# Optimization experiments

Hardware: AMD Instinct MI355X
Metric: run time of the kernel (lower is better)

Reference implementation:

```python
import jax, jax.numpy as jnp
import numpy as np

AH, AW = 7, 7            # alignedHeight, alignedWidth
SCALE = 0.0625           # spatialScale = 1/16


def setup_inputs() -> dict:
    key = jax.random.key(0)
    k1, k2, k3, k4 = jax.random.split(key, 4)
    B, C, H, W, K = 4, 1024, 50, 50, 512
    features = jax.random.normal(k1, (B, C, H, W), dtype=jnp.float32)
    bidx = jax.random.randint(k2, (K, 1), 0, B).astype(jnp.float32)
    xs = jnp.sort(jax.random.uniform(k3, (K, 2), minval=0.0, maxval=799.0), axis=1)
    ys = jnp.sort(jax.random.uniform(k4, (K, 2), minval=0.0, maxval=799.0), axis=1)
    # rois: (batch_idx, x1, y1, x2, y2) in image coords
    rois = jnp.concatenate([bidx, xs[:, 0:1], ys[:, 0:1], xs[:, 1:2], ys[:, 1:2]], axis=1)
    return {"features": features, "rois": rois}


def _roi_align(features, rois):
    # legacy roi_align: grid of (AH+1)x(AW+1) points, bin = extent/(grid-1),
    # one bilinear sample per grid point, zero outside feature map.
    B, C, H, W = features.shape
    bidx = rois[:, 0].astype(jnp.int32)
    x1 = rois[:, 1] * SCALE
    y1 = rois[:, 2] * SCALE
    x2 = rois[:, 3] * SCALE
    y2 = rois[:, 4] * SCALE
    bh = jnp.maximum(y2 - y1, 0.0) / AH  # (AH+1)-1 grid intervals
    bw = jnp.maximum(x2 - x1, 0.0) / AW
    ys = y1[:, None] + jnp.arange(AH + 1, dtype=jnp.float32) * bh[:, None]  # [K,AH+1]
    xs = x1[:, None] + jnp.arange(AW + 1, dtype=jnp.float32) * bw[:, None]  # [K,AW+1]
    yg = ys[:, :, None]   # [K,AH+1,1]
    xg = xs[:, None, :]   # [K,1,AW+1]
    valid = (yg >= 0) & (yg < H) & (xg >= 0) & (xg < W)   # [K,AH+1,AW+1]
    y0 = jnp.clip(jnp.floor(yg), 0, H - 2).astype(jnp.int32)
    x0 = jnp.clip(jnp.floor(xg), 0, W - 2).astype(jnp.int32)
    wy = yg - y0.astype(jnp.float32)  # [K,AH+1,1]
    wx = xg - x0.astype(jnp.float32)  # [K,1,AW+1]
    b = bidx[:, None, None]
    # gathered corners: [K, AH+1, AW+1, C]
    v00 = features[b, :, y0, x0]
    v01 = features[b, :, y0, x0 + 1]
    v10 = features[b, :, y0 + 1, x0]
    v11 = features[b, :, y0 + 1, x0 + 1]
    out = (v00 * ((1 - wy) * (1 - wx))[..., None]
           + v01 * ((1 - wy) * wx)[..., None]
           + v10 * (wy * (1 - wx))[..., None]
           + v11 * (wy * wx)[..., None])
    out = jnp.where(valid[..., None], out, 0.0)
    return jnp.transpose(out, (0, 3, 1, 2))  # [K, C, AH+1, AW+1]


def reference(features, rois):
    a = _roi_align(features, rois)
    # avg_pool2d(kernel=2, stride=1) -> [K, C, AH, AW]
    pooled = (a[..., :-1, :-1] + a[..., 1:, :-1] + a[..., :-1, 1:] + a[..., 1:, 1:]) * 0.25
    return pooled
```

## Files before the change

kernel.cpp:

```cpp
#include <hip/hip_runtime.h>

#define K_ROIS   512
#define BATCH    4
#define CHANNELS 1024
#define FH       50
#define FW       50
#define AH       7
#define AW       7
#define SCALE_F  0.0625f
#define CPT      4


__global__ void roi_prep(const float* __restrict__ rois,
                         int* __restrict__ cnt,
                         int* __restrict__ list,
                         float4* __restrict__ params) {
    int r = blockIdx.x * blockDim.x + threadIdx.x;
    if (r >= K_ROIS) return;
    float bf = rois[r * 5 + 0];
    float x1 = rois[r * 5 + 1] * SCALE_F;
    float y1 = rois[r * 5 + 2] * SCALE_F;
    float x2 = rois[r * 5 + 3] * SCALE_F;
    float y2 = rois[r * 5 + 4] * SCALE_F;
    float bw = fmaxf(x2 - x1, 0.f) * (1.f / (float)AW);
    float bh = fmaxf(y2 - y1, 0.f) * (1.f / (float)AH);
    params[r] = make_float4(x1, y1, bw, bh);
    int ib = (int)bf;
    int pos = atomicAdd(&cnt[ib], 1);
    list[ib * K_ROIS + pos] = r;
}

__global__ __launch_bounds__(256)
void roi_pool(const float* __restrict__ feat,
              const int* __restrict__ cnt,
              const int* __restrict__ list,
              const float4* __restrict__ params,
              float* __restrict__ out) {
    __shared__ float4 patch4[CPT * FH * FW / 4];
    float* patch = (float*)patch4;

    const int b  = blockIdx.x & 3;
    const int c0 = (blockIdx.x >> 2) * CPT;

    const float4* src = (const float4*)(feat + ((size_t)b * CHANNELS + c0) * (FH * FW));
    for (int idx = threadIdx.x; idx < CPT * FH * FW / 4; idx += 256)
        patch4[idx] = src[idx];
    __syncthreads();

    const int lane = threadIdx.x & 63;
    const int wv   = threadIdx.x >> 6;
    const int j = lane >> 3;
    const int i = lane & 7;
    const float jf = (float)j;
    const float iff = (float)i;
    const bool do_out = (j < AH) && (i < AW);
    const int outoff = j * AW + i;

    const int n = cnt[b];
    for (int rr = wv; rr < n; rr += 4) {
        const int roi = list[b * K_ROIS + rr];
        const float4 p = params[roi];
        const float xg = fmaf(iff, p.z, p.x);
        const float yg = fmaf(jf, p.w, p.y);
        const bool valid = (yg >= 0.f) && (yg < (float)FH) &&
                           (xg >= 0.f) && (xg < (float)FW);
        const float y0f = fminf(fmaxf(floorf(yg), 0.f), (float)(FH - 2));
        const float x0f = fminf(fmaxf(floorf(xg), 0.f), (float)(FW - 2));
        const float wy = yg - y0f;
        const float wx = xg - x0f;
        const float omwy = 1.f - wy;
        const float omwx = 1.f - wx;
        float w00 = omwy * omwx;
        float w01 = omwy * wx;
        float w10 = wy * omwx;
        float w11 = wy * wx;
        if (!valid) { w00 = 0.f; w01 = 0.f; w10 = 0.f; w11 = 0.f; }
        const int addr = (int)y0f * FW + (int)x0f;
        const size_t obase = (size_t)roi * (CHANNELS * AH * AW)
                           + (size_t)c0 * (AH * AW) + outoff;
        #pragma unroll
        for (int ch = 0; ch < CPT; ++ch) {
            const int a = ch * (FH * FW) + addr;
            const float v00 = patch[a];
            const float v01 = patch[a + 1];
            const float v10 = patch[a + FW];
            const float v11 = patch[a + FW + 1];
            float s = w00 * v00 + w01 * v01 + w10 * v10 + w11 * v11;
            float s1 = s + __shfl_down(s, 1);
            float s2 = s1 + __shfl_down(s1, 8);
            if (do_out)
                out[obase + (size_t)ch * (AH * AW)] = s2 * 0.25f;
        }
    }
}

extern "C" void kernel_launch(void* const* d_in, const int* in_sizes, int n_in,
                              void* d_out, int out_size, void* d_ws, size_t ws_size,
                              hipStream_t stream) {
    const float* feat = (const float*)d_in[0];
    const float* rois = (const float*)d_in[1];
    float* out = (float*)d_out;

    char* ws = (char*)d_ws;
    int* cnt      = (int*)ws;
    int* list     = (int*)(ws + 16);
    float4* params = (float4*)(ws + 16 + 4 * K_ROIS * sizeof(int));

    hipMemsetAsync(cnt, 0, 16, stream);
    roi_prep<<<2, 256, 0, stream>>>(rois, cnt, list, params);
    roi_pool<<<BATCH * (CHANNELS / CPT), 256, 0, stream>>>(feat, cnt, list, params, out);
}
```

Baseline: 160.2 us.

## Interleave channels in shared patch as float4 and prefetch sorted ROI params

The shared-memory patch is now stored channel-interleaved as one float4 per pixel, so each bilinear corner is a single 128-bit LDS read covering all four channels instead of four scalar reads. ROI parameters are written directly in per-batch sorted order by the prep kernel, removing the indirect params[roi] lookup, and the next ROI's parameters are software-prefetched one iteration ahead. The global load into shared memory becomes four scalar strided loads per pixel instead of coalesced float4 loads, which may cost more on the staging side. Workspace usage grows because params are now sized per batch slot.

```diff
diff --git a/kernel.cpp b/kernel.cpp
--- a/kernel.cpp
+++ b/kernel.cpp
@@ -13,8 +13,8 @@
 
 __global__ void roi_prep(const float* __restrict__ rois,
                          int* __restrict__ cnt,
-                         int* __restrict__ list,
-                         float4* __restrict__ params) {
+                         int* __restrict__ roiIdx,
+                         float4* __restrict__ paramsS) {
     int r = blockIdx.x * blockDim.x + threadIdx.x;
     if (r >= K_ROIS) return;
     float bf = rois[r * 5 + 0];
@@ -24,27 +24,32 @@
     float y2 = rois[r * 5 + 4] * SCALE_F;
     float bw = fmaxf(x2 - x1, 0.f) * (1.f / (float)AW);
     float bh = fmaxf(y2 - y1, 0.f) * (1.f / (float)AH);
-    params[r] = make_float4(x1, y1, bw, bh);
     int ib = (int)bf;
     int pos = atomicAdd(&cnt[ib], 1);
-    list[ib * K_ROIS + pos] = r;
+    roiIdx[ib * K_ROIS + pos] = r;
+    paramsS[ib * K_ROIS + pos] = make_float4(x1, y1, bw, bh);
 }
 
 __global__ __launch_bounds__(256)
 void roi_pool(const float* __restrict__ feat,
               const int* __restrict__ cnt,
-              const int* __restrict__ list,
-              const float4* __restrict__ params,
+              const int* __restrict__ roiIdx,
+              const float4* __restrict__ paramsS,
               float* __restrict__ out) {
-    __shared__ float4 patch4[CPT * FH * FW / 4];
-    float* patch = (float*)patch4;
+    __shared__ float4 patch4[FH * FW];
 
     const int b  = blockIdx.x & 3;
     const int c0 = (blockIdx.x >> 2) * CPT;
 
-    const float4* src = (const float4*)(feat + ((size_t)b * CHANNELS + c0) * (FH * FW));
-    for (int idx = threadIdx.x; idx < CPT * FH * FW / 4; idx += 256)
-        patch4[idx] = src[idx];
+    const float* pl = feat + ((size_t)b * CHANNELS + c0) * (FH * FW);
+    for (int idx = threadIdx.x; idx < FH * FW; idx += 256) {
+        float4 v;
+        v.x = pl[idx];
+        v.y = pl[idx + FH * FW];
+        v.z = pl[idx + 2 * FH * FW];
+        v.w = pl[idx + 3 * FH * FW];
+        patch4[idx] = v;
+    }
     __syncthreads();
 
     const int lane = threadIdx.x & 63;
@@ -57,11 +62,21 @@
     const int outoff = j * AW + i;
 
     const int n = cnt[b];
-    for (int rr = wv; rr < n; rr += 4) {
-        const int roi = list[b * K_ROIS + rr];
-        const float4 p = params[roi];
-        const float xg = fmaf(iff, p.z, p.x);
-        const float yg = fmaf(jf, p.w, p.y);
+    const int base = b * K_ROIS;
+
+    int rr = wv;
+    float4 pp = make_float4(0.f, 0.f, 0.f, 0.f);
+    int roi = 0;
+    if (rr < n) { pp = paramsS[base + rr]; roi = roiIdx[base + rr]; }
+
+    while (rr < n) {
+        const int rn = rr + 4;
+        float4 ppn = pp;
+        int roin = roi;
+        if (rn < n) { ppn = paramsS[base + rn]; roin = roiIdx[base + rn]; }
+
+        const float xg = fmaf(iff, pp.z, pp.x);
+        const float yg = fmaf(jf, pp.w, pp.y);
         const bool valid = (yg >= 0.f) && (yg < (float)FH) &&
                            (xg >= 0.f) && (xg < (float)FW);
         const float y0f = fminf(fmaxf(floorf(yg), 0.f), (float)(FH - 2));
@@ -75,22 +90,39 @@
         float w10 = wy * omwx;
         float w11 = wy * wx;
         if (!valid) { w00 = 0.f; w01 = 0.f; w10 = 0.f; w11 = 0.f; }
-        const int addr = (int)y0f * FW + (int)x0f;
-        const size_t obase = (size_t)roi * (CHANNELS * AH * AW)
-                           + (size_t)c0 * (AH * AW) + outoff;
-        #pragma unroll
-        for (int ch = 0; ch < CPT; ++ch) {
-            const int a = ch * (FH * FW) + addr;
-            const float v00 = patch[a];
-            const float v01 = patch[a + 1];
-            const float v10 = patch[a + FW];
-            const float v11 = patch[a + FW + 1];
-            float s = w00 * v00 + w01 * v01 + w10 * v10 + w11 * v11;
-            float s1 = s + __shfl_down(s, 1);
-            float s2 = s1 + __shfl_down(s1, 8);
-            if (do_out)
-                out[obase + (size_t)ch * (AH * AW)] = s2 * 0.25f;
+        const int p = (int)y0f * FW + (int)x0f;
+
+        const float4 c00 = patch4[p];
+        const float4 c01 = patch4[p + 1];
+        const float4 c10 = patch4[p + FW];
+        const float4 c11 = patch4[p + FW + 1];
+
+        float4 s;
+        s.x = w00 * c00.x + w01 * c01.x + w10 * c10.x + w11 * c11.x;
+        s.y = w00 * c00.y + w01 * c01.y + w10 * c10.y + w11 * c11.y;
+        s.z = w00 * c00.z + w01 * c01.z + w10 * c10.z + w11 * c11.z;
+        s.w = w00 * c00.w + w01 * c01.w + w10 * c10.w + w11 * c11.w;
+
+        float4 t;
+        t.x = s.x + __shfl_down(s.x, 1);
+        t.y = s.y + __shfl_down(s.y, 1);
+        t.z = s.z + __shfl_down(s.z, 1);
+        t.w = s.w + __shfl_down(s.w, 1);
+        t.x += __shfl_down(t.x, 8);
+        t.y += __shfl_down(t.y, 8);
+        t.z += __shfl_down(t.z, 8);
+        t.w += __shfl_down(t.w, 8);
+
+        if (do_out) {
+            const size_t ob = (size_t)roi * (CHANNELS * AH * AW)
+                            + (size_t)c0 * (AH * AW) + outoff;
+            out[ob]                = t.x * 0.25f;
+            out[ob + AH * AW]      = t.y * 0.25f;
+            out[ob + 2 * AH * AW]  = t.z * 0.25f;
+            out[ob + 3 * AH * AW]  = t.w * 0.25f;
         }
+
+        pp = ppn; roi = roin; rr = rn;
     }
 }
 
@@ -102,11 +134,11 @@
     float* out = (float*)d_out;
 
     char* ws = (char*)d_ws;
-    int* cnt      = (int*)ws;
-    int* list     = (int*)(ws + 16);
-    float4* params = (float4*)(ws + 16 + 4 * K_ROIS * sizeof(int));
+    int* cnt        = (int*)ws;
+    int* roiIdx     = (int*)(ws + 16);
+    float4* paramsS = (float4*)(ws + 16 + 4 * K_ROIS * sizeof(int));
 
     hipMemsetAsync(cnt, 0, 16, stream);
-    roi_prep<<<2, 256, 0, stream>>>(rois, cnt, list, params);
-    roi_pool<<<BATCH * (CHANNELS / CPT), 256, 0, stream>>>(feat, cnt, list, params, out);
+    roi_prep<<<2, 256, 0, stream>>>(rois, cnt, roiIdx, paramsS);
+    roi_pool<<<BATCH * (CHANNELS / CPT), 256, 0, stream>>>(feat, cnt, roiIdx, paramsS, out);
 }
```

After: 152.0 us. 5.1% less time.
